# Performance work log

Hardware: AMD Instinct MI355X
Metric: run time of the kernel (lower is better)

Reference implementation:

```python
import jax, jax.numpy as jnp
import numpy as np

EPS = 1e-5

def setup_inputs() -> dict:
    key = jax.random.key(0)
    ks = jax.random.split(key, 4)
    B, C, A, T = 32, 1536, 128, 1000  # batch, in_channels, attention_channels, time
    x = jax.random.normal(ks[0], (B, C, T), dtype=jnp.float32)
    # attention MLP: Conv1d(3C -> A, k=1) -> ReLU -> BN(A) -> Conv1d(A -> C, k=1)
    w1 = jax.random.normal(ks[1], (A, 3 * C), dtype=jnp.float32) / np.float32(np.sqrt(3 * C))
    b1 = jnp.zeros((A,), jnp.float32)
    g1 = jnp.ones((A,), jnp.float32)
    be1 = jnp.zeros((A,), jnp.float32)
    rm1 = jnp.zeros((A,), jnp.float32)
    rv1 = jnp.ones((A,), jnp.float32)
    w2 = jax.random.normal(ks[2], (C, A), dtype=jnp.float32) / np.float32(np.sqrt(A))
    b2 = jnp.zeros((C,), jnp.float32)
    # final BatchNorm1d over 2C pooled features
    g2 = jnp.ones((2 * C,), jnp.float32)
    be2 = jnp.zeros((2 * C,), jnp.float32)
    rm2 = jnp.zeros((2 * C,), jnp.float32)
    rv2 = jnp.ones((2 * C,), jnp.float32)
    return {"x": x, "w1": w1, "b1": b1, "g1": g1, "be1": be1, "rm1": rm1, "rv1": rv1,
            "w2": w2, "b2": b2, "g2": g2, "be2": be2, "rm2": rm2, "rv2": rv2}

def reference(x, w1, b1, g1, be1, rm1, rv1, w2, b2, g2, be2, rm2, rv2):
    # x: [B, C, T]
    mean_x = jnp.mean(x, axis=2, keepdims=True)                       # [B,C,1]
    std_x = jnp.sqrt(jnp.var(x, axis=2, ddof=1, keepdims=True) + EPS)  # unbiased var
    cat = jnp.concatenate([x,
                           jnp.broadcast_to(mean_x, x.shape),
                           jnp.broadcast_to(std_x, x.shape)], axis=1)  # [B,3C,T]
    # conv1x1 == channel matmul
    h = jnp.einsum('ac,bct->bat', w1, cat) + b1[None, :, None]         # [B,A,T]
    h = jax.nn.relu(h)
    # BatchNorm1d(A), inference mode with running stats
    h = (h - rm1[None, :, None]) * (g1 / jnp.sqrt(rv1 + EPS))[None, :, None] + be1[None, :, None]
    logits = jnp.einsum('ca,bat->bct', w2, h) + b2[None, :, None]      # [B,C,T]
    attn = jax.nn.softmax(logits, axis=2)
    xs = x * attn
    mu = jnp.sum(xs, axis=2)                                           # [B,C]
    sum_sq = jnp.sum(xs * x, axis=2)                                   # [B,C]
    sigma = jnp.sqrt(jnp.abs(sum_sq - mu ** 2) + EPS)
    pool = jnp.concatenate([mu, sigma], axis=1)                        # [B,2C]
    # final BatchNorm1d(2C), inference mode
    return (pool - rm2) * (g2 / jnp.sqrt(rv2 + EPS)) + be2
```

## Files before the change

### kernel.cpp

```cpp
#include <hip/hip_runtime.h>
#include <hip/hip_bf16.h>

#define BATCH 32
#define CCH   1536
#define ACH   128
#define TLEN  1000
#define TPAD  1024
#define NCB   (CCH / 64)
#define XTB   (TPAD * 64)
#define TSPLIT 4
#define TCHUNK 256
#define TSA   2
#define EPSV  1e-5f
#define NINF  -3.0e38f
#define LOG2E 1.4426950408889634f
#define RTHR  11.5f

typedef __attribute__((ext_vector_type(8))) short bf16x8;
typedef __attribute__((ext_vector_type(4))) float f32x4;

__device__ __forceinline__ unsigned short f2bf(float f) {
    union { float f; unsigned u; } v; v.f = f;
    unsigned r = v.u + 0x7fffu + ((v.u >> 16) & 1u);
    return (unsigned short)(r >> 16);
}
__device__ __forceinline__ float bf2f(unsigned short u) {
    union { unsigned u; float f; } v; v.u = ((unsigned)u) << 16;
    return v.f;
}

__global__ __launch_bounds__(512) void kA(const float* __restrict__ x,
                                          unsigned short* __restrict__ xt,
                                          float* __restrict__ st1,
                                          float* __restrict__ st2) {
    int b = blockIdx.y, cblk = blockIdx.x, ts = blockIdx.z;
    int cb = cblk * 64;
    int tbase = ts * (TPAD / TSA);
    int tid = threadIdx.x;
    int row = tid >> 3, l8 = tid & 7;
    __shared__ float tile[2][64][65];
    __shared__ float red1[8][64], red2[8][64];
    const float* xr = x + ((size_t)(b * CCH + cb + row)) * TLEN + tbase;
    unsigned short* xtp = xt + ((size_t)(b * NCB + cblk)) * XTB + (size_t)tbase * 64;

    float4 rA[2];
    float cs1[8], cs2[8];
    #pragma unroll
    for (int j = 0; j < 8; ++j) { cs1[j] = 0.f; cs2[j] = 0.f; }

    auto loadTile = [&](int it) {
        #pragma unroll
        for (int p = 0; p < 2; ++p) {
            int tf = it * 64 + p * 32 + l8 * 4;
            float4 vv = make_float4(0.f, 0.f, 0.f, 0.f);
            if (tbase + tf < TLEN) vv = *reinterpret_cast<const float4*>(xr + tf);
            rA[p] = vv;
        }
    };
    auto writeTile = [&](int buf) {
        #pragma unroll
        for (int p = 0; p < 2; ++p) {
            int tl = p * 32 + l8 * 4;
            tile[buf][tl + 0][row] = rA[p].x;
            tile[buf][tl + 1][row] = rA[p].y;
            tile[buf][tl + 2][row] = rA[p].z;
            tile[buf][tl + 3][row] = rA[p].w;
        }
    };
    auto readStore = [&](int buf, int it) {
        int tl = tid >> 3;
        int c8 = (tid & 7) * 8;
        float v[8];
        #pragma unroll
        for (int j = 0; j < 8; ++j) {
            v[j] = tile[buf][tl][c8 + j];
            cs1[j] += v[j];
            cs2[j] += v[j] * v[j];
        }
        unsigned o[4];
        #pragma unroll
        for (int j = 0; j < 4; ++j)
            o[j] = (unsigned)f2bf(v[2 * j]) | ((unsigned)f2bf(v[2 * j + 1]) << 16);
        uint4 u; u.x = o[0]; u.y = o[1]; u.z = o[2]; u.w = o[3];
        *reinterpret_cast<uint4*>(xtp + (size_t)(it * 64 + tl) * 64 + c8) = u;
    };

    const int NIT = (TPAD / TSA) / 64;
    loadTile(0);
    writeTile(0);
    loadTile(1);
    __syncthreads();
    for (int it = 0; it < NIT; ++it) {
        int buf = it & 1;
        if (it < NIT - 1) writeTile(buf ^ 1);
        if (it < NIT - 2) loadTile(it + 2);
        readStore(buf, it);
        __syncthreads();
    }

    #pragma unroll
    for (int j = 0; j < 8; ++j) {
        #pragma unroll
        for (int d = 8; d < 64; d <<= 1) {
            cs1[j] += __shfl_xor(cs1[j], d);
            cs2[j] += __shfl_xor(cs2[j], d);
        }
    }
    int wv = tid >> 6, lane = tid & 63;
    if (lane < 8) {
        #pragma unroll
        for (int j = 0; j < 8; ++j) {
            red1[wv][lane * 8 + j] = cs1[j];
            red2[wv][lane * 8 + j] = cs2[j];
        }
    }
    __syncthreads();
    if (tid < 64) {
        float s1 = 0.f, s2 = 0.f;
        #pragma unroll
        for (int w = 0; w < 8; ++w) { s1 += red1[w][tid]; s2 += red2[w][tid]; }
        st1[((size_t)ts * BATCH + b) * CCH + cb + tid] = s1;
        st2[((size_t)ts * BATCH + b) * CCH + cb + tid] = s2;
    }
}

__global__ __launch_bounds__(256) void kAm(const float* __restrict__ st1,
                                           const float* __restrict__ st2,
                                           float* __restrict__ meanw,
                                           float* __restrict__ stdw) {
    int idx = blockIdx.x * 256 + threadIdx.x;
    float s1 = st1[idx] + st1[(size_t)BATCH * CCH + idx];
    float s2 = st2[idx] + st2[(size_t)BATCH * CCH + idx];
    float mean = s1 / (float)TLEN;
    float var = (s2 - s1 * s1 / (float)TLEN) / (float)(TLEN - 1);
    meanw[idx] = mean;
    stdw[idx] = sqrtf(var + EPSV);
}

__global__ __launch_bounds__(256) void kA2(const float* __restrict__ x,
                                           float* __restrict__ meanw,
                                           float* __restrict__ stdw) {
    int b = blockIdx.y, cb = blockIdx.x * 32;
    int tid = threadIdx.x;
    int row = tid >> 3, l8 = tid & 7;
    const float* xr = x + ((size_t)(b * CCH + cb + row)) * TLEN;
    float s1 = 0.f, s2 = 0.f;
    for (int tf = l8 * 4; tf < TLEN; tf += 32) {
        float4 vv = *reinterpret_cast<const float4*>(xr + tf);
        s1 += vv.x + vv.y + vv.z + vv.w;
        s2 += vv.x * vv.x + vv.y * vv.y + vv.z * vv.z + vv.w * vv.w;
    }
    #pragma unroll
    for (int d = 1; d < 8; d <<= 1) { s1 += __shfl_xor(s1, d); s2 += __shfl_xor(s2, d); }
    if (l8 == 0) {
        float mean = s1 / (float)TLEN;
        float var = (s2 - s1 * s1 / (float)TLEN) / (float)(TLEN - 1);
        meanw[b * CCH + cb + row] = mean;
        stdw[b * CCH + cb + row] = sqrtf(var + EPSV);
    }
}

__global__ __launch_bounds__(256) void kBW(const float* __restrict__ w1,
                                           unsigned short* __restrict__ w1x,
                                           const float* __restrict__ w2,
                                           const float* __restrict__ b2,
                                           const float* __restrict__ g1,
                                           const float* __restrict__ be1,
                                           const float* __restrict__ rm1,
                                           const float* __restrict__ rv1,
                                           unsigned short* __restrict__ w2e,
                                           float* __restrict__ b2e) {
    int bx = blockIdx.x;
    const int NB1 = (ACH * CCH) / 256;
    if (bx < NB1) {
        int e = bx * 256 + threadIdx.x;
        int a = e / CCH, c = e - a * CCH;
        w1x[e] = f2bf(w1[(size_t)a * (3 * CCH) + c]);
    } else {
        int c = (bx - NB1) * 4 + (threadIdx.x >> 6);
        int l = threadIdx.x & 63;
        float acc = 0.f;
        #pragma unroll
        for (int p = 0; p < 2; ++p) {
            int a = p * 64 + l;
            float s1 = g1[a] * rsqrtf(rv1[a] + EPSV);
            float w = w2[(size_t)c * ACH + a];
            w2e[(size_t)c * ACH + a] = f2bf(w * s1 * LOG2E);
            acc += w * (be1[a] - s1 * rm1[a]);
        }
        #pragma unroll
        for (int d = 1; d < 64; d <<= 1) acc += __shfl_xor(acc, d);
        if (l == 0) b2e[c] = (b2[c] + acc) * LOG2E;
    }
}

__global__ __launch_bounds__(64) void kB2(const float* __restrict__ w1,
                                          const float* __restrict__ b1,
                                          const float* __restrict__ meanw,
                                          const float* __restrict__ stdw,
                                          float* __restrict__ hbias) {
    int a = blockIdx.x, b = blockIdx.y, l = threadIdx.x;
    const float* wr = w1 + (size_t)a * 3 * CCH;
    const float* mb = meanw + b * CCH;
    const float* sb = stdw + b * CCH;
    float acc = 0.f;
    for (int k = l; k < CCH; k += 64)
        acc += wr[CCH + k] * mb[k] + wr[2 * CCH + k] * sb[k];
    #pragma unroll
    for (int d = 1; d < 64; d <<= 1) acc += __shfl_xor(acc, d);
    if (l == 0) hbias[b * ACH + a] = acc + b1[a];
}

__global__ __launch_bounds__(512) void kC3(const unsigned short* __restrict__ xt,
                                           const unsigned short* __restrict__ w1x,
                                           const float* __restrict__ hbias,
                                           unsigned short* __restrict__ h) {
    int b = blockIdx.y;
    int t0 = blockIdx.x * 64;
    int tid = threadIdx.x;
    int wv = tid >> 6, l = tid & 63, g = l >> 4, r = l & 15;
    int a0 = (wv & 3) * 32;
    int tw = (wv >> 2) * 32;

    __shared__ uint4 As[2][1024];
    __shared__ uint4 Bs[2][512];

    const unsigned short* bG = xt + (size_t)b * NCB * XTB;

    int qa0 = tid, qa1 = tid + 512, qb = tid;
    int wa0 = qa0 ^ ((qa0 >> 3) & 7), wa1 = qa1 ^ ((qa1 >> 3) & 7), wb = qb ^ ((qb >> 3) & 7);
    int arow0 = qa0 >> 3, arow1 = qa1 >> 3, acol = (qa0 & 7) * 8;
    int brow = qb >> 3, bcol = (qb & 7) * 8;

    As[0][wa0] = *reinterpret_cast<const uint4*>(w1x + (size_t)arow0 * CCH + acol);
    As[0][wa1] = *reinterpret_cast<const uint4*>(w1x + (size_t)arow1 * CCH + acol);
    Bs[0][wb]  = *reinterpret_cast<const uint4*>(bG + (size_t)(t0 + brow) * 64 + bcol);
    __syncthreads();

    f32x4 acc[2][2];
    #pragma unroll
    for (int i = 0; i < 2; ++i)
        #pragma unroll
        for (int j = 0; j < 2; ++j) acc[i][j] = f32x4{0.f, 0.f, 0.f, 0.f};

    for (int ks = 0; ks < CCH / 64; ++ks) {
        int buf = ks & 1;
        uint4 na0, na1, nb;
        if (ks < CCH / 64 - 1) {
            int cofs = (ks + 1) * 64;
            na0 = *reinterpret_cast<const uint4*>(w1x + (size_t)arow0 * CCH + cofs + acol);
            na1 = *reinterpret_cast<const uint4*>(w1x + (size_t)arow1 * CCH + cofs + acol);
            nb  = *reinterpret_cast<const uint4*>(bG + (size_t)(ks + 1) * XTB + (size_t)(t0 + brow) * 64 + bcol);
        }
        bf16x8 Af[2][2], Bf[2][2];
        #pragma unroll
        for (int at = 0; at < 2; ++at) {
            int row = a0 + 16 * at + r;
            #pragma unroll
            for (int kk = 0; kk < 2; ++kk) {
                int ch = (row * 8 + kk * 4 + g) ^ (row & 7);
                Af[at][kk] = *reinterpret_cast<const bf16x8*>(&As[buf][ch]);
            }
        }
        #pragma unroll
        for (int tt = 0; tt < 2; ++tt) {
            int row = tw + 16 * tt + r;
            #pragma unroll
            for (int kk = 0; kk < 2; ++kk) {
                int ch = (row * 8 + kk * 4 + g) ^ (row & 7);
                Bf[tt][kk] = *reinterpret_cast<const bf16x8*>(&Bs[buf][ch]);
            }
        }
        #pragma unroll
        for (int kk = 0; kk < 2; ++kk)
            #pragma unroll
            for (int at = 0; at < 2; ++at)
                #pragma unroll
                for (int tt = 0; tt < 2; ++tt)
                    acc[at][tt] = __builtin_amdgcn_mfma_f32_16x16x32_bf16(Af[at][kk], Bf[tt][kk], acc[at][tt], 0, 0, 0);
        if (ks < CCH / 64 - 1) {
            As[buf ^ 1][wa0] = na0;
            As[buf ^ 1][wa1] = na1;
            Bs[buf ^ 1][wb]  = nb;
        }
        __syncthreads();
    }

    #pragma unroll
    for (int at = 0; at < 2; ++at) {
        f32x4 hb = *reinterpret_cast<const f32x4*>(hbias + b * ACH + a0 + 16 * at + 4 * g);
        #pragma unroll
        for (int tt = 0; tt < 2; ++tt) {
            int t = t0 + tw + 16 * tt + r;
            float v0 = acc[at][tt][0] + hb[0]; v0 = v0 > 0.f ? v0 : 0.f;
            float v1 = acc[at][tt][1] + hb[1]; v1 = v1 > 0.f ? v1 : 0.f;
            float v2 = acc[at][tt][2] + hb[2]; v2 = v2 > 0.f ? v2 : 0.f;
            float v3 = acc[at][tt][3] + hb[3]; v3 = v3 > 0.f ? v3 : 0.f;
            uint2 u;
            u.x = (unsigned)f2bf(v0) | ((unsigned)f2bf(v1) << 16);
            u.y = (unsigned)f2bf(v2) | ((unsigned)f2bf(v3) << 16);
            *reinterpret_cast<uint2*>(h + ((size_t)(b * TPAD + t)) * ACH + a0 + 16 * at + 4 * g) = u;
        }
    }
}

__global__ __launch_bounds__(256) void kC2(const float* __restrict__ x,
                                           const unsigned short* __restrict__ w1x,
                                           const float* __restrict__ hbias,
                                           unsigned short* __restrict__ h) {
    int b = blockIdx.y;
    int t0 = blockIdx.x * 32;
    int tid = threadIdx.x;
    int wv = tid >> 6, l = tid & 63, g = l >> 4, r = l & 15;
    const unsigned short* aptr = w1x + (size_t)(32 * wv + r) * CCH + 8 * g;
    f32x4 acc[2][2];
    #pragma unroll
    for (int i = 0; i < 2; ++i)
        #pragma unroll
        for (int j = 0; j < 2; ++j) acc[i][j] = f32x4{0.f, 0.f, 0.f, 0.f};
    for (int kk = 0; kk < CCH / 32; ++kk) {
        bf16x8 Af[2], Bf[2];
        #pragma unroll
        for (int at = 0; at < 2; ++at)
            Af[at] = *reinterpret_cast<const bf16x8*>(aptr + (size_t)(16 * at) * CCH + 32 * kk);
        #pragma unroll
        for (int tt = 0; tt < 2; ++tt) {
            int t = t0 + 16 * tt + r;
            unsigned short tmp[8];
            #pragma unroll
            for (int j = 0; j < 8; ++j) {
                float xv = 0.f;
                if (t < TLEN) xv = x[((size_t)(b * CCH + 32 * kk + 8 * g + j)) * TLEN + t];
                tmp[j] = f2bf(xv);
            }
            Bf[tt] = *reinterpret_cast<const bf16x8*>(tmp);
        }
        #pragma unroll
        for (int at = 0; at < 2; ++at)
            #pragma unroll
            for (int tt = 0; tt < 2; ++tt)
                acc[at][tt] = __builtin_amdgcn_mfma_f32_16x16x32_bf16(Af[at], Bf[tt], acc[at][tt], 0, 0, 0);
    }
    #pragma unroll
    for (int at = 0; at < 2; ++at) {
        f32x4 hb = *reinterpret_cast<const f32x4*>(hbias + b * ACH + 32 * wv + 16 * at + 4 * g);
        #pragma unroll
        for (int tt = 0; tt < 2; ++tt) {
            int t = t0 + 16 * tt + r;
            float v0 = acc[at][tt][0] + hb[0]; v0 = v0 > 0.f ? v0 : 0.f;
            float v1 = acc[at][tt][1] + hb[1]; v1 = v1 > 0.f ? v1 : 0.f;
            float v2 = acc[at][tt][2] + hb[2]; v2 = v2 > 0.f ? v2 : 0.f;
            float v3 = acc[at][tt][3] + hb[3]; v3 = v3 > 0.f ? v3 : 0.f;
            uint2 u;
            u.x = (unsigned)f2bf(v0) | ((unsigned)f2bf(v1) << 16);
            u.y = (unsigned)f2bf(v2) | ((unsigned)f2bf(v3) << 16);
            *reinterpret_cast<uint2*>(h + ((size_t)(b * TPAD + t)) * ACH + 32 * wv + 16 * at + 4 * g) = u;
        }
    }
}

__global__ __launch_bounds__(256) void kD3(const unsigned short* __restrict__ xt,
                                           const unsigned short* __restrict__ h,
                                           const unsigned short* __restrict__ w2e,
                                           const float* __restrict__ b2e,
                                           float4* __restrict__ part) {
    int b = blockIdx.y, ts = blockIdx.z;
    int cblk = blockIdx.x * 128;
    int tid = threadIdx.x;
    int wv = tid >> 6, l = tid & 63, g = l >> 4, r = l & 15;
    int c0 = cblk + 32 * wv;
    int t0 = ts * TCHUNK;

    __shared__ uint4 hs[2][512];

    bf16x8 W[2][4];
    f32x4 b2v[2];
    #pragma unroll
    for (int af = 0; af < 2; ++af) {
        #pragma unroll
        for (int kk = 0; kk < 4; ++kk)
            W[af][kk] = *reinterpret_cast<const bf16x8*>(w2e + (size_t)(c0 + 16 * af + r) * ACH + 32 * kk + 8 * g);
        b2v[af] = *reinterpret_cast<const f32x4*>(b2e + c0 + 16 * af + 4 * g);
    }

    const unsigned short* hbase = h + (size_t)(b * TPAD + t0) * ACH;
    const unsigned short* xb = xt + (size_t)b * NCB * XTB;
    const unsigned short* xp[2];
    #pragma unroll
    for (int af = 0; af < 2; ++af) {
        int cAbs = c0 + 16 * af + 4 * g;
        xp[af] = xb + (size_t)(cAbs >> 6) * XTB + (cAbs & 63);
    }

    int q0 = tid, q1 = tid + 256;
    int w0 = q0 ^ ((q0 >> 4) & 7), w1 = q1 ^ ((q1 >> 4) & 7);

    hs[0][w0] = *reinterpret_cast<const uint4*>(hbase + q0 * 8);
    hs[0][w1] = *reinterpret_cast<const uint4*>(hbase + q1 * 8);
    __syncthreads();

    float m[2][4], s[2][4], wx[2][4], wxx[2][4];
    #pragma unroll
    for (int af = 0; af < 2; ++af)
        #pragma unroll
        for (int i = 0; i < 4; ++i) { m[af][i] = NINF; s[af][i] = 0.f; wx[af][i] = 0.f; wxx[af][i] = 0.f; }

    for (int tc = 0; tc < TCHUNK / 32; ++tc) {
        int buf = tc & 1;
        uint4 n0, n1;
        if (tc < TCHUNK / 32 - 1) {
            const unsigned short* src = hbase + (size_t)(tc + 1) * 32 * ACH;
            n0 = *reinterpret_cast<const uint4*>(src + q0 * 8);
            n1 = *reinterpret_cast<const uint4*>(src + q1 * 8);
        }
        int tb0 = t0 + tc * 32 + r, tb1 = tb0 + 16;
        uint2 xu[2][2];
        #pragma unroll
        for (int af = 0; af < 2; ++af) {
            xu[af][0] = *reinterpret_cast<const uint2*>(xp[af] + (size_t)tb0 * 64);
            xu[af][1] = *reinterpret_cast<const uint2*>(xp[af] + (size_t)tb1 * 64);
        }

        f32x4 a2[2][2];
        a2[0][0] = f32x4{0.f, 0.f, 0.f, 0.f}; a2[0][1] = f32x4{0.f, 0.f, 0.f, 0.f};
        a2[1][0] = f32x4{0.f, 0.f, 0.f, 0.f}; a2[1][1] = f32x4{0.f, 0.f, 0.f, 0.f};
        #pragma unroll
        for (int tt = 0; tt < 2; ++tt) {
            int tl = tt * 16 + r;
            #pragma unroll
            for (int kk = 0; kk < 4; ++kk) {
                int ch = (tl * 16 + kk * 4 + g) ^ (tl & 7);
                bf16x8 Bf = *reinterpret_cast<const bf16x8*>(&hs[buf][ch]);
                a2[0][tt] = __builtin_amdgcn_mfma_f32_16x16x32_bf16(W[0][kk], Bf, a2[0][tt], 0, 0, 0);
                a2[1][tt] = __builtin_amdgcn_mfma_f32_16x16x32_bf16(W[1][kk], Bf, a2[1][tt], 0, 0, 0);
            }
        }

        bool val0 = (tb0 < TLEN), val1 = (tb1 < TLEN);
        #pragma unroll
        for (int af = 0; af < 2; ++af) {
            float xv0[4], xv1[4];
            xv0[0] = bf2f((unsigned short)(xu[af][0].x & 0xffff));
            xv0[1] = bf2f((unsigned short)(xu[af][0].x >> 16));
            xv0[2] = bf2f((unsigned short)(xu[af][0].y & 0xffff));
            xv0[3] = bf2f((unsigned short)(xu[af][0].y >> 16));
            xv1[0] = bf2f((unsigned short)(xu[af][1].x & 0xffff));
            xv1[1] = bf2f((unsigned short)(xu[af][1].x >> 16));
            xv1[2] = bf2f((unsigned short)(xu[af][1].y & 0xffff));
            xv1[3] = bf2f((unsigned short)(xu[af][1].y >> 16));
            #pragma unroll
            for (int i = 0; i < 4; ++i) {
                float v0 = val0 ? (a2[af][0][i] + b2v[af][i]) : NINF;
                float v1 = val1 ? (a2[af][1][i] + b2v[af][i]) : NINF;
                float mx = fmaxf(v0, v1);
                if (__any(mx > m[af][i] + RTHR)) {
                    float mn = fmaxf(m[af][i], mx);
                    float sc = exp2f(m[af][i] - mn);
                    s[af][i] *= sc; wx[af][i] *= sc; wxx[af][i] *= sc; m[af][i] = mn;
                }
                float e0 = exp2f(v0 - m[af][i]);
                float e1 = exp2f(v1 - m[af][i]);
                float xe0 = xv0[i] * e0, xe1 = xv1[i] * e1;
                s[af][i]   += e0 + e1;
                wx[af][i]  += xe0 + xe1;
                wxx[af][i] += xv0[i] * xe0 + xv1[i] * xe1;
            }
        }

        if (tc < TCHUNK / 32 - 1) {
            hs[buf ^ 1][w0] = n0;
            hs[buf ^ 1][w1] = n1;
        }
        __syncthreads();
    }

    #pragma unroll
    for (int af = 0; af < 2; ++af)
        #pragma unroll
        for (int i = 0; i < 4; ++i) {
            float mm = m[af][i], ss = s[af][i], sx = wx[af][i], sxx = wxx[af][i];
            #pragma unroll
            for (int d = 1; d < 16; d <<= 1) {
                float mo = __shfl_xor(mm, d);
                float so = __shfl_xor(ss, d);
                float xo = __shfl_xor(sx, d);
                float qo = __shfl_xor(sxx, d);
                float mn = fmaxf(mm, mo);
                float fa = exp2f(mm - mn), fb = exp2f(mo - mn);
                ss = ss * fa + so * fb;
                sx = sx * fa + xo * fb;
                sxx = sxx * fa + qo * fb;
                mm = mn;
            }
            if (r == 0) {
                int c = c0 + 16 * af + 4 * g + i;
                float4 p; p.x = mm; p.y = ss; p.z = sx; p.w = sxx;
                part[((size_t)(b * TSPLIT + ts)) * CCH + c] = p;
            }
        }
}

__global__ __launch_bounds__(256) void kD1(const float* __restrict__ x,
                                           const unsigned short* __restrict__ h,
                                           const unsigned short* __restrict__ w2e,
                                           const float* __restrict__ b2e,
                                           float4* __restrict__ part) {
    int b = blockIdx.y, ts = blockIdx.z;
    int cblk = blockIdx.x * 64;
    int tid = threadIdx.x;
    int wv = tid >> 6, l = tid & 63, g = l >> 4, r = l & 15;
    int c0 = cblk + 16 * wv;
    int t0 = ts * TCHUNK;
    __shared__ float xs[2][64][36];

    bf16x8 W[4];
    #pragma unroll
    for (int kk = 0; kk < 4; ++kk)
        W[kk] = *reinterpret_cast<const bf16x8*>(w2e + (size_t)(c0 + r) * ACH + 32 * kk + 8 * g);
    f32x4 b2v = *reinterpret_cast<const f32x4*>(b2e + c0 + 4 * g);

    int sc_ = tid >> 2;
    int st_ = (tid & 3) * 8;
    const float* xrow = x + ((size_t)(b * CCH + cblk + sc_)) * TLEN;
    const unsigned short* hb = h + (size_t)(b * TPAD) * ACH + 8 * g;

    auto stage = [&](int buf, int tc) {
        int tg = t0 + tc * 32;
        #pragma unroll
        for (int p = 0; p < 2; ++p) {
            int tl = st_ + 4 * p;
            float4 v = make_float4(0.f, 0.f, 0.f, 0.f);
            if (tg + tl < TLEN) v = *reinterpret_cast<const float4*>(xrow + tg + tl);
            *reinterpret_cast<float4*>(&xs[buf][sc_][tl]) = v;
        }
    };

    float m[4], s[4], wx[4], wxx[4];
    #pragma unroll
    for (int i = 0; i < 4; ++i) { m[i] = NINF; s[i] = 0.f; wx[i] = 0.f; wxx[i] = 0.f; }

    stage(0, 0);
    __syncthreads();
    for (int tc = 0; tc < TCHUNK / 32; ++tc) {
        int buf = tc & 1;
        if (tc + 1 < TCHUNK / 32) stage(buf ^ 1, tc + 1);
        f32x4 a2[2];
        a2[0] = f32x4{0.f, 0.f, 0.f, 0.f};
        a2[1] = f32x4{0.f, 0.f, 0.f, 0.f};
        #pragma unroll
        for (int tt = 0; tt < 2; ++tt) {
            int t = t0 + tc * 32 + tt * 16 + r;
            #pragma unroll
            for (int kk = 0; kk < 4; ++kk) {
                bf16x8 Bf = *reinterpret_cast<const bf16x8*>(hb + (size_t)t * ACH + 32 * kk);
                a2[tt] = __builtin_amdgcn_mfma_f32_16x16x32_bf16(W[kk], Bf, a2[tt], 0, 0, 0);
            }
        }
        int tb = t0 + tc * 32 + r;
        bool val0 = (tb < TLEN), val1 = (tb + 16 < TLEN);
        #pragma unroll
        for (int i = 0; i < 4; ++i) {
            int cl = 16 * wv + 4 * g + i;
            float v0 = val0 ? (a2[0][i] + b2v[i]) : NINF;
            float v1 = val1 ? (a2[1][i] + b2v[i]) : NINF;
            float mx = fmaxf(v0, v1);
            if (mx > m[i] + RTHR) {
                float sc = exp2f(m[i] - mx);
                s[i] *= sc; wx[i] *= sc; wxx[i] *= sc; m[i] = mx;
            }
            float e0 = exp2f(v0 - m[i]);
            float e1 = exp2f(v1 - m[i]);
            float x0 = xs[buf][cl][r];
            float x1 = xs[buf][cl][r + 16];
            float xe0 = x0 * e0, xe1 = x1 * e1;
            s[i]   += e0 + e1;
            wx[i]  += xe0 + xe1;
            wxx[i] += x0 * xe0 + x1 * xe1;
        }
        __syncthreads();
    }

    #pragma unroll
    for (int i = 0; i < 4; ++i) {
        float mm = m[i], ss = s[i], sx = wx[i], sxx = wxx[i];
        #pragma unroll
        for (int d = 1; d < 16; d <<= 1) {
            float mo = __shfl_xor(mm, d);
            float so = __shfl_xor(ss, d);
            float xo = __shfl_xor(sx, d);
            float qo = __shfl_xor(sxx, d);
            float mn = fmaxf(mm, mo);
            float fa = exp2f(mm - mn), fb = exp2f(mo - mn);
            ss = ss * fa + so * fb;
            sx = sx * fa + xo * fb;
            sxx = sxx * fa + qo * fb;
            mm = mn;
        }
        if (r == 0) {
            int c = c0 + 4 * g + i;
            float4 p; p.x = mm; p.y = ss; p.z = sx; p.w = sxx;
            part[((size_t)(b * TSPLIT + ts)) * CCH + c] = p;
        }
    }
}

__global__ __launch_bounds__(256) void kE(const float4* __restrict__ part,
                                          const float* __restrict__ rm2,
                                          const float* __restrict__ rv2,
                                          const float* __restrict__ g2,
                                          const float* __restrict__ be2,
                                          float* __restrict__ out) {
    int idx = blockIdx.x * 256 + threadIdx.x;
    int b = idx / CCH, c = idx - b * CCH;
    float m = NINF, s = 0.f, wx = 0.f, wxx = 0.f;
    #pragma unroll
    for (int ts = 0; ts < TSPLIT; ++ts) {
        float4 p = part[((size_t)(b * TSPLIT + ts)) * CCH + c];
        float mn = fmaxf(m, p.x);
        float fa = exp2f(m - mn), fb = exp2f(p.x - mn);
        s = s * fa + p.y * fb;
        wx = wx * fa + p.z * fb;
        wxx = wxx * fa + p.w * fb;
        m = mn;
    }
    float mu = wx / s;
    float ssq = wxx / s;
    float sig = sqrtf(fabsf(ssq - mu * mu) + EPSV);
    out[b * 2 * CCH + c] = (mu - rm2[c]) * g2[c] * rsqrtf(rv2[c] + EPSV) + be2[c];
    int c2 = CCH + c;
    out[b * 2 * CCH + c2] = (sig - rm2[c2]) * g2[c2] * rsqrtf(rv2[c2] + EPSV) + be2[c2];
}

extern "C" void kernel_launch(void* const* d_in, const int* in_sizes, int n_in,
                              void* d_out, int out_size, void* d_ws, size_t ws_size,
                              hipStream_t stream) {
    const float* x   = (const float*)d_in[0];
    const float* w1  = (const float*)d_in[1];
    const float* b1  = (const float*)d_in[2];
    const float* g1  = (const float*)d_in[3];
    const float* be1 = (const float*)d_in[4];
    const float* rm1 = (const float*)d_in[5];
    const float* rv1 = (const float*)d_in[6];
    const float* w2  = (const float*)d_in[7];
    const float* b2  = (const float*)d_in[8];
    const float* g2  = (const float*)d_in[9];
    const float* be2 = (const float*)d_in[10];
    const float* rm2 = (const float*)d_in[11];
    const float* rv2 = (const float*)d_in[12];
    float* out = (float*)d_out;

    const size_t sz_xt    = (size_t)BATCH * NCB * XTB * 2;
    const size_t sz_h     = (size_t)BATCH * TPAD * ACH * 2;
    const size_t sz_w1x   = (size_t)ACH * CCH * 2;
    const size_t sz_w2e   = (size_t)CCH * ACH * 2;
    const size_t sz_mean  = (size_t)BATCH * CCH * 4;
    const size_t sz_std   = sz_mean;
    const size_t sz_st    = (size_t)TSA * BATCH * CCH * 4;
    const size_t sz_hbias = (size_t)BATCH * ACH * 4;
    const size_t sz_b2e   = (size_t)CCH * 4;
    const size_t sz_part  = (size_t)BATCH * TSPLIT * CCH * 16;
    const size_t need_small = sz_h + sz_w1x + sz_w2e + sz_mean + sz_std + 2 * sz_st
                            + sz_hbias + sz_b2e + sz_part;
    bool use_xt = (ws_size >= need_small + sz_xt);

    char* ws = (char*)d_ws;
    unsigned short* xt = nullptr;
    if (use_xt) { xt = (unsigned short*)ws; ws += sz_xt; }
    unsigned short* hbuf = (unsigned short*)ws; ws += sz_h;
    unsigned short* w1x  = (unsigned short*)ws; ws += sz_w1x;
    unsigned short* w2e  = (unsigned short*)ws; ws += sz_w2e;
    float* meanw = (float*)ws; ws += sz_mean;
    float* stdw  = (float*)ws; ws += sz_std;
    float* st1   = (float*)ws; ws += sz_st;
    float* st2   = (float*)ws; ws += sz_st;
    float* hbias = (float*)ws; ws += sz_hbias;
    float* b2e   = (float*)ws; ws += sz_b2e;
    float4* part = (float4*)ws; ws += sz_part;

    const int NBW = (ACH * CCH) / 256 + CCH / 4;
    if (use_xt) {
        kA<<<dim3(NCB, BATCH, TSA), 512, 0, stream>>>(x, xt, st1, st2);
        kBW<<<NBW, 256, 0, stream>>>(w1, w1x, w2, b2, g1, be1, rm1, rv1, w2e, b2e);
        kAm<<<(BATCH * CCH) / 256, 256, 0, stream>>>(st1, st2, meanw, stdw);
    } else {
        kA2<<<dim3(48, 32), 256, 0, stream>>>(x, meanw, stdw);
        kBW<<<NBW, 256, 0, stream>>>(w1, w1x, w2, b2, g1, be1, rm1, rv1, w2e, b2e);
    }
    kB2<<<dim3(ACH, BATCH), 64, 0, stream>>>(w1, b1, meanw, stdw, hbias);
    if (use_xt) {
        kC3<<<dim3(TPAD / 64, BATCH), 512, 0, stream>>>(xt, w1x, hbias, hbuf);
        kD3<<<dim3(CCH / 128, BATCH, TSPLIT), 256, 0, stream>>>(xt, hbuf, w2e, b2e, part);
    } else {
        kC2<<<dim3(TPAD / 32, BATCH), 256, 0, stream>>>(x, w1x, hbias, hbuf);
        kD1<<<dim3(CCH / 64, BATCH, TSPLIT), 256, 0, stream>>>(x, hbuf, w2e, b2e, part);
    }
    kE<<<(BATCH * CCH) / 256, 256, 0, stream>>>(part, rm2, rv2, g2, be2, out);
}
```

Baseline: 149.8 us.

## Stage x tiles through LDS in pooling kernel and fold stats finalize into bias kernel

The pooling kernel now loads the bf16 transposed x panel with coalesced 16-byte loads into a swizzled, double-buffered LDS tile alongside h. Previously each lane issued scattered 8-byte global loads per timestep, and these were not prefetched. Separately, the mean/std finalize kernel is removed and the computation moved into the hbias kernel, which reads the raw partial sums directly. This saves one launch and one round trip through global memory, but the hbias kernel now recomputes sqrt for each channel in every attention row (128x redundancy) and kD4 needs more LDS per block.

Result: faster. 143.7 us (median of 3 runs) (-4.1%).

```diff
diff --git a/kernel.cpp b/kernel.cpp
--- a/kernel.cpp
+++ b/kernel.cpp
@@ -124,22 +124,9 @@
     }
 }
 
-__global__ __launch_bounds__(256) void kAm(const float* __restrict__ st1,
-                                           const float* __restrict__ st2,
-                                           float* __restrict__ meanw,
-                                           float* __restrict__ stdw) {
-    int idx = blockIdx.x * 256 + threadIdx.x;
-    float s1 = st1[idx] + st1[(size_t)BATCH * CCH + idx];
-    float s2 = st2[idx] + st2[(size_t)BATCH * CCH + idx];
-    float mean = s1 / (float)TLEN;
-    float var = (s2 - s1 * s1 / (float)TLEN) / (float)(TLEN - 1);
-    meanw[idx] = mean;
-    stdw[idx] = sqrtf(var + EPSV);
-}
-
 __global__ __launch_bounds__(256) void kA2(const float* __restrict__ x,
-                                           float* __restrict__ meanw,
-                                           float* __restrict__ stdw) {
+                                           float* __restrict__ st1,
+                                           float* __restrict__ st2) {
     int b = blockIdx.y, cb = blockIdx.x * 32;
     int tid = threadIdx.x;
     int row = tid >> 3, l8 = tid & 7;
@@ -153,10 +140,11 @@
     #pragma unroll
     for (int d = 1; d < 8; d <<= 1) { s1 += __shfl_xor(s1, d); s2 += __shfl_xor(s2, d); }
     if (l8 == 0) {
-        float mean = s1 / (float)TLEN;
-        float var = (s2 - s1 * s1 / (float)TLEN) / (float)(TLEN - 1);
-        meanw[b * CCH + cb + row] = mean;
-        stdw[b * CCH + cb + row] = sqrtf(var + EPSV);
+        int idx = b * CCH + cb + row;
+        st1[idx] = s1;
+        st2[idx] = s2;
+        st1[(size_t)BATCH * CCH + idx] = 0.f;
+        st2[(size_t)BATCH * CCH + idx] = 0.f;
     }
 }
 
@@ -194,18 +182,27 @@
     }
 }
 
-__global__ __launch_bounds__(64) void kB2(const float* __restrict__ w1,
-                                          const float* __restrict__ b1,
-                                          const float* __restrict__ meanw,
-                                          const float* __restrict__ stdw,
-                                          float* __restrict__ hbias) {
+__global__ __launch_bounds__(64) void kB2n(const float* __restrict__ w1,
+                                           const float* __restrict__ b1,
+                                           const float* __restrict__ st1,
+                                           const float* __restrict__ st2,
+                                           float* __restrict__ hbias) {
     int a = blockIdx.x, b = blockIdx.y, l = threadIdx.x;
     const float* wr = w1 + (size_t)a * 3 * CCH;
-    const float* mb = meanw + b * CCH;
-    const float* sb = stdw + b * CCH;
+    const float* p1 = st1 + (size_t)b * CCH;
+    const float* p2 = st2 + (size_t)b * CCH;
+    const size_t half = (size_t)BATCH * CCH;
     float acc = 0.f;
-    for (int k = l; k < CCH; k += 64)
-        acc += wr[CCH + k] * mb[k] + wr[2 * CCH + k] * sb[k];
+    const float invT = 1.f / (float)TLEN;
+    const float invT1 = 1.f / (float)(TLEN - 1);
+    for (int k = l; k < CCH; k += 64) {
+        float s1 = p1[k] + p1[half + k];
+        float s2 = p2[k] + p2[half + k];
+        float mean = s1 * invT;
+        float var = (s2 - s1 * s1 * invT) * invT1;
+        float stdv = sqrtf(var + EPSV);
+        acc += wr[CCH + k] * mean + wr[2 * CCH + k] * stdv;
+    }
     #pragma unroll
     for (int d = 1; d < 64; d <<= 1) acc += __shfl_xor(acc, d);
     if (l == 0) hbias[b * ACH + a] = acc + b1[a];
@@ -359,7 +356,7 @@
     }
 }
 
-__global__ __launch_bounds__(256) void kD3(const unsigned short* __restrict__ xt,
+__global__ __launch_bounds__(256) void kD4(const unsigned short* __restrict__ xt,
                                            const unsigned short* __restrict__ h,
                                            const unsigned short* __restrict__ w2e,
                                            const float* __restrict__ b2e,
@@ -372,6 +369,7 @@
     int t0 = ts * TCHUNK;
 
     __shared__ uint4 hs[2][512];
+    __shared__ uint2 xs[2][1024];
 
     bf16x8 W[2][4];
     f32x4 b2v[2];
@@ -384,19 +382,38 @@
     }
 
     const unsigned short* hbase = h + (size_t)(b * TPAD + t0) * ACH;
-    const unsigned short* xb = xt + (size_t)b * NCB * XTB;
-    const unsigned short* xp[2];
-    #pragma unroll
-    for (int af = 0; af < 2; ++af) {
-        int cAbs = c0 + 16 * af + 4 * g;
-        xp[af] = xb + (size_t)(cAbs >> 6) * XTB + (cAbs & 63);
-    }
+    const unsigned short* xpan = xt + ((size_t)b * NCB + (cblk >> 6)) * XTB;
 
     int q0 = tid, q1 = tid + 256;
     int w0 = q0 ^ ((q0 >> 4) & 7), w1 = q1 ^ ((q1 >> 4) & 7);
-
-    hs[0][w0] = *reinterpret_cast<const uint4*>(hbase + q0 * 8);
-    hs[0][w1] = *reinterpret_cast<const uint4*>(hbase + q1 * 8);
+    int xtl = tid >> 3, xw7 = tid & 7;
+    int xc0 = (xtl * 16 + xw7) ^ (xtl & 7);
+    int xc1 = (xtl * 16 + 8 + xw7) ^ (xtl & 7);
+    int xg[2];
+    #pragma unroll
+    for (int af = 0; af < 2; ++af) {
+        int gx = 8 * wv + 4 * af + g;
+        xg[af] = (r * 32 + gx) ^ ((r & 7) << 1);
+    }
+
+    auto ldH = [&](int tc, uint4& a, uint4& bq) {
+        const unsigned short* src = hbase + (size_t)tc * 32 * ACH;
+        a  = *reinterpret_cast<const uint4*>(src + q0 * 8);
+        bq = *reinterpret_cast<const uint4*>(src + q1 * 8);
+    };
+    auto ldX = [&](int tc, uint4& a, uint4& bq) {
+        size_t off = (size_t)(t0 + tc * 32 + xtl) * 64 + xw7 * 8;
+        a  = *reinterpret_cast<const uint4*>(xpan + off);
+        bq = *reinterpret_cast<const uint4*>(xpan + XTB + off);
+    };
+
+    {
+        uint4 h0, h1, x0, x1;
+        ldH(0, h0, h1); ldX(0, x0, x1);
+        hs[0][w0] = h0; hs[0][w1] = h1;
+        *reinterpret_cast<uint4*>(&xs[0][2 * xc0]) = x0;
+        *reinterpret_cast<uint4*>(&xs[0][2 * xc1]) = x1;
+    }
     __syncthreads();
 
     float m[2][4], s[2][4], wx[2][4], wxx[2][4];
@@ -407,18 +424,10 @@
 
     for (int tc = 0; tc < TCHUNK / 32; ++tc) {
         int buf = tc & 1;
-        uint4 n0, n1;
+        uint4 nh0, nh1, nx0, nx1;
         if (tc < TCHUNK / 32 - 1) {
-            const unsigned short* src = hbase + (size_t)(tc + 1) * 32 * ACH;
-            n0 = *reinterpret_cast<const uint4*>(src + q0 * 8);
-            n1 = *reinterpret_cast<const uint4*>(src + q1 * 8);
-        }
-        int tb0 = t0 + tc * 32 + r, tb1 = tb0 + 16;
-        uint2 xu[2][2];
-        #pragma unroll
-        for (int af = 0; af < 2; ++af) {
-            xu[af][0] = *reinterpret_cast<const uint2*>(xp[af] + (size_t)tb0 * 64);
-            xu[af][1] = *reinterpret_cast<const uint2*>(xp[af] + (size_t)tb1 * 64);
+            ldH(tc + 1, nh0, nh1);
+            ldX(tc + 1, nx0, nx1);
         }
 
         f32x4 a2[2][2];
@@ -436,18 +445,21 @@
             }
         }
 
+        int tb0 = t0 + tc * 32 + r, tb1 = tb0 + 16;
         bool val0 = (tb0 < TLEN), val1 = (tb1 < TLEN);
         #pragma unroll
         for (int af = 0; af < 2; ++af) {
+            uint2 xu0 = xs[buf][xg[af]];
+            uint2 xu1 = xs[buf][xg[af] + 512];
             float xv0[4], xv1[4];
-            xv0[0] = bf2f((unsigned short)(xu[af][0].x & 0xffff));
-            xv0[1] = bf2f((unsigned short)(xu[af][0].x >> 16));
-            xv0[2] = bf2f((unsigned short)(xu[af][0].y & 0xffff));
-            xv0[3] = bf2f((unsigned short)(xu[af][0].y >> 16));
-            xv1[0] = bf2f((unsigned short)(xu[af][1].x & 0xffff));
-            xv1[1] = bf2f((unsigned short)(xu[af][1].x >> 16));
-            xv1[2] = bf2f((unsigned short)(xu[af][1].y & 0xffff));
-            xv1[3] = bf2f((unsigned short)(xu[af][1].y >> 16));
+            xv0[0] = bf2f((unsigned short)(xu0.x & 0xffff));
+            xv0[1] = bf2f((unsigned short)(xu0.x >> 16));
+            xv0[2] = bf2f((unsigned short)(xu0.y & 0xffff));
+            xv0[3] = bf2f((unsigned short)(xu0.y >> 16));
+            xv1[0] = bf2f((unsigned short)(xu1.x & 0xffff));
+            xv1[1] = bf2f((unsigned short)(xu1.x >> 16));
+            xv1[2] = bf2f((unsigned short)(xu1.y & 0xffff));
+            xv1[3] = bf2f((unsigned short)(xu1.y >> 16));
             #pragma unroll
             for (int i = 0; i < 4; ++i) {
                 float v0 = val0 ? (a2[af][0][i] + b2v[af][i]) : NINF;
@@ -468,8 +480,10 @@
         }
 
         if (tc < TCHUNK / 32 - 1) {
-            hs[buf ^ 1][w0] = n0;
-            hs[buf ^ 1][w1] = n1;
+            hs[buf ^ 1][w0] = nh0;
+            hs[buf ^ 1][w1] = nh1;
+            *reinterpret_cast<uint4*>(&xs[buf ^ 1][2 * xc0]) = nx0;
+            *reinterpret_cast<uint4*>(&xs[buf ^ 1][2 * xc1]) = nx1;
         }
         __syncthreads();
     }
@@ -511,7 +525,7 @@
     int wv = tid >> 6, l = tid & 63, g = l >> 4, r = l & 15;
     int c0 = cblk + 16 * wv;
     int t0 = ts * TCHUNK;
-    __shared__ float xs[2][64][36];
+    __shared__ float xsf[2][64][36];
 
     bf16x8 W[4];
     #pragma unroll
@@ -531,7 +545,7 @@
             int tl = st_ + 4 * p;
             float4 v = make_float4(0.f, 0.f, 0.f, 0.f);
             if (tg + tl < TLEN) v = *reinterpret_cast<const float4*>(xrow + tg + tl);
-            *reinterpret_cast<float4*>(&xs[buf][sc_][tl]) = v;
+            *reinterpret_cast<float4*>(&xsf[buf][sc_][tl]) = v;
         }
     };
 
@@ -570,8 +584,8 @@
             }
             float e0 = exp2f(v0 - m[i]);
             float e1 = exp2f(v1 - m[i]);
-            float x0 = xs[buf][cl][r];
-            float x1 = xs[buf][cl][r + 16];
+            float x0 = xsf[buf][cl][r];
+            float x1 = xsf[buf][cl][r + 16];
             float xe0 = x0 * e0, xe1 = x1 * e1;
             s[i]   += e0 + e1;
             wx[i]  += xe0 + xe1;
@@ -653,13 +667,11 @@
     const size_t sz_h     = (size_t)BATCH * TPAD * ACH * 2;
     const size_t sz_w1x   = (size_t)ACH * CCH * 2;
     const size_t sz_w2e   = (size_t)CCH * ACH * 2;
-    const size_t sz_mean  = (size_t)BATCH * CCH * 4;
-    const size_t sz_std   = sz_mean;
     const size_t sz_st    = (size_t)TSA * BATCH * CCH * 4;
     const size_t sz_hbias = (size_t)BATCH * ACH * 4;
     const size_t sz_b2e   = (size_t)CCH * 4;
     const size_t sz_part  = (size_t)BATCH * TSPLIT * CCH * 16;
-    const size_t need_small = sz_h + sz_w1x + sz_w2e + sz_mean + sz_std + 2 * sz_st
+    const size_t need_small = sz_h + sz_w1x + sz_w2e + 2 * sz_st
                             + sz_hbias + sz_b2e + sz_part;
     bool use_xt = (ws_size >= need_small + sz_xt);
 
@@ -669,8 +681,6 @@
     unsigned short* hbuf = (unsigned short*)ws; ws += sz_h;
     unsigned short* w1x  = (unsigned short*)ws; ws += sz_w1x;
     unsigned short* w2e  = (unsigned short*)ws; ws += sz_w2e;
-    float* meanw = (float*)ws; ws += sz_mean;
-    float* stdw  = (float*)ws; ws += sz_std;
     float* st1   = (float*)ws; ws += sz_st;
     float* st2   = (float*)ws; ws += sz_st;
     float* hbias = (float*)ws; ws += sz_hbias;
@@ -678,18 +688,15 @@
     float4* part = (float4*)ws; ws += sz_part;
 
     const int NBW = (ACH * CCH) / 256 + CCH / 4;
-    if (use_xt) {
+    if (use_xt)
         kA<<<dim3(NCB, BATCH, TSA), 512, 0, stream>>>(x, xt, st1, st2);
-        kBW<<<NBW, 256, 0, stream>>>(w1, w1x, w2, b2, g1, be1, rm1, rv1, w2e, b2e);
-        kAm<<<(BATCH * CCH) / 256, 256, 0, stream>>>(st1, st2, meanw, stdw);
-    } else {
-        kA2<<<dim3(48, 32), 256, 0, stream>>>(x, meanw, stdw);
-        kBW<<<NBW, 256, 0, stream>>>(w1, w1x, w2, b2, g1, be1, rm1, rv1, w2e, b2e);
-    }
-    kB2<<<dim3(ACH, BATCH), 64, 0, stream>>>(w1, b1, meanw, stdw, hbias);
+    else
+        kA2<<<dim3(48, 32), 256, 0, stream>>>(x, st1, st2);
+    kBW<<<NBW, 256, 0, stream>>>(w1, w1x, w2, b2, g1, be1, rm1, rv1, w2e, b2e);
+    kB2n<<<dim3(ACH, BATCH), 64, 0, stream>>>(w1, b1, st1, st2, hbias);
     if (use_xt) {
         kC3<<<dim3(TPAD / 64, BATCH), 512, 0, stream>>>(xt, w1x, hbias, hbuf);
-        kD3<<<dim3(CCH / 128, BATCH, TSPLIT), 256, 0, stream>>>(xt, hbuf, w2e, b2e, part);
+        kD4<<<dim3(CCH / 128, BATCH, TSPLIT), 256, 0, stream>>>(xt, hbuf, w2e, b2e, part);
     } else {
         kC2<<<dim3(TPAD / 32, BATCH), 256, 0, stream>>>(x, w1x, hbias, hbuf);
         kD1<<<dim3(CCH / 64, BATCH, TSPLIT), 256, 0, stream>>>(x, hbuf, w2e, b2e, part);
```
